# Kernel tuning notes

Measured on AMD Instinct MI355X. Metric: run time of the kernel, lower is better.

The kernel has to match this reference:

```python
import jax, jax.numpy as jnp
import numpy as np

B, NVEC, DIM, HEADS, DH, M, ITERS, DEPTH, NCLASS, KER = 8, 4096, 512, 8, 64, 256, 6, 2, 10, 33
INNER = HEADS * DH


def _ln(x, g, b, eps=1e-5):
    mu = x.mean(-1, keepdims=True)
    var = ((x - mu) ** 2).mean(-1, keepdims=True)
    return (x - mu) * jax.lax.rsqrt(var + eps) * g + b


def _mp_pinv(x, iters=ITERS):
    # Moore-Penrose pseudo-inverse via Newton-Schulz iterations (lucidrains).
    # x: [b, h, m, m]
    abs_x = jnp.abs(x)
    col = abs_x.sum(-1).max(-1)  # [b, h]
    row = abs_x.sum(-2).max(-1)  # [b, h]
    z = jnp.swapaxes(x, -1, -2) / (col * row)[..., None, None]
    I = jnp.eye(x.shape[-1], dtype=x.dtype)
    for _ in range(iters):
        xz = x @ z
        z = 0.25 * z @ (13.0 * I - xz @ (15.0 * I - xz @ (7.0 * I - xz)))
    return z


def _nystrom_attn(x, qkv_w, out_w, out_b, conv_w):
    b, n, _ = x.shape
    qkv = x @ qkv_w  # [b, n, 3*inner]
    q, k, v = jnp.split(qkv, 3, axis=-1)
    to_h = lambda t: t.reshape(b, n, HEADS, DH).transpose(0, 2, 1, 3)  # [b,h,n,dh]
    q, k, v = to_h(q), to_h(k), to_h(v)
    q = q * (DH ** -0.5)

    l = n // M  # tokens per landmark segment (n divisible by M)
    q_l = q.reshape(b, HEADS, M, l, DH).mean(3)  # [b,h,M,dh]
    k_l = k.reshape(b, HEADS, M, l, DH).mean(3)

    attn1 = jax.nn.softmax(jnp.einsum('bhnd,bhmd->bhnm', q, k_l), axis=-1)    # [b,h,n,M]
    attn2 = jax.nn.softmax(jnp.einsum('bhmd,bhld->bhml', q_l, k_l), axis=-1)  # [b,h,M,M]
    attn3 = jax.nn.softmax(jnp.einsum('bhmd,bhnd->bhmn', q_l, k), axis=-1)    # [b,h,M,n]

    out = (attn1 @ _mp_pinv(attn2)) @ (attn3 @ v)  # [b,h,n,dh]

    # residual depthwise conv over sequence dim (kernel 33, groups=heads, no bias)
    out = out + jax.lax.conv_general_dilated(
        v, conv_w, (1, 1), [(KER // 2, KER // 2), (0, 0)],
        dimension_numbers=('NCHW', 'OIHW', 'NCHW'), feature_group_count=HEADS)

    out = out.transpose(0, 2, 1, 3).reshape(b, n, INNER)
    return out @ out_w + out_b


def setup_inputs():
    key = jax.random.key(0)
    ks = jax.random.split(key, 12)
    s = 0.02
    f32 = jnp.float32
    return {
        'x': jax.random.normal(ks[0], (B, NVEC, 2), f32),
        'lin_w': jax.random.normal(ks[1], (2, DIM), f32) * s,
        'lin_b': jnp.zeros((DIM,), f32),
        'ln1_g': jnp.ones((DEPTH, DIM), f32),
        'ln1_b': jnp.zeros((DEPTH, DIM), f32),
        'qkv_w': jax.random.normal(ks[2], (DEPTH, DIM, 3 * INNER), f32) * s,
        'out_w': jax.random.normal(ks[3], (DEPTH, INNER, DIM), f32) * s,
        'out_b': jnp.zeros((DEPTH, DIM), f32),
        'conv_w': jax.random.normal(ks[4], (DEPTH, HEADS, 1, KER, 1), f32) * s,
        'ln2_g': jnp.ones((DEPTH, DIM), f32),
        'ln2_b': jnp.zeros((DEPTH, DIM), f32),
        'ff1_w': jax.random.normal(ks[5], (DEPTH, DIM, 4 * DIM), f32) * s,
        'ff1_b': jnp.zeros((DEPTH, 4 * DIM), f32),
        'ff2_w': jax.random.normal(ks[6], (DEPTH, 4 * DIM, DIM), f32) * s,
        'ff2_b': jnp.zeros((DEPTH, DIM), f32),
        'final_w': jax.random.normal(ks[7], (NVEC * DIM, NCLASS), f32) * s,
        'final_b': jnp.zeros((NCLASS,), f32),
    }


def reference(x, lin_w, lin_b, ln1_g, ln1_b, qkv_w, out_w, out_b, conv_w,
              ln2_g, ln2_b, ff1_w, ff1_b, ff2_w, ff2_b, final_w, final_b):
    h = x @ lin_w + lin_b  # [B, NVEC, DIM]
    for i in range(DEPTH):
        h = h + _nystrom_attn(_ln(h, ln1_g[i], ln1_b[i]), qkv_w[i], out_w[i], out_b[i], conv_w[i])
        z = _ln(h, ln2_g[i], ln2_b[i])
        h = h + (jax.nn.gelu(z @ ff1_w[i] + ff1_b[i]) @ ff2_w[i] + ff2_b[i])
    return h.reshape(h.shape[0], -1) @ final_w + final_b  # [B, NCLASS]
```

## Files before the change

### kernel.cpp

```cpp
#include <hip/hip_runtime.h>
#include <hip/hip_bf16.h>

#define BB_ 8
#define NVEC 4096
#define DIM 512
#define HEADS 8
#define DH 64
#define MM_ 256
#define ITERS 6
#define DEPTH 2
#define NCLASS 10
#define KER 33
#define INNER 512
#define LSEG 16

typedef long long ll;
typedef __bf16 bh16;
typedef __attribute__((ext_vector_type(8))) __bf16 bf16x8;
typedef __attribute__((ext_vector_type(4))) float f32x4;

template<int WR, int WC, bool TRB, bool GELU_ACT, bool RESID, bool BF16OUT,
         bool DUAL, bool SMAX>
__global__ void __launch_bounds__(256)
mgemm_k(const bh16* __restrict__ A, const bh16* __restrict__ B,
        const float* __restrict__ bias, void* __restrict__ Cv, void* __restrict__ C2v,
        int K, int lda, int ldb, int ldc,
        int BI, ll sAo, ll sAi, ll sBo, ll sBi, ll sCo, ll sCi,
        float alpha, float diagv)
{
    constexpr int BM = WR * 64, BN = WC * 64;
    const int bz = blockIdx.z;
    const int bo = bz / BI, bi = bz % BI;
    const bh16* Ab = A + bo * sAo + (ll)bi * sAi;
    const bh16* Bb = B + bo * sBo + (ll)bi * sBi;
    const ll coff = bo * sCo + (ll)bi * sCi;

    const int gx = gridDim.x;
    const int nwg = gx * gridDim.y;
    int flat = blockIdx.y * gx + blockIdx.x;
    {
        int xcd = flat & 7, base = flat >> 3;
        int q = nwg >> 3, rr = nwg & 7;
        flat = (xcd < rr ? xcd * (q + 1) : rr * (q + 1) + (xcd - rr) * q) + base;
    }
    const int m0 = (flat / gx) * BM;
    const int n0 = (flat % gx) * BN;

    const int tid = threadIdx.x;
    const int lane = tid & 63;
    const int wave = tid >> 6;
    const int wr = wave / WC, wc = wave % WC;

    __shared__ bh16 Al[BM * 32];
    __shared__ bh16 Bl[BN * 32];
    __shared__ float srow[SMAX ? 4 * 64 : 4];

    f32x4 acc[4][4];
#pragma unroll
    for (int i = 0; i < 4; ++i)
#pragma unroll
        for (int j = 0; j < 4; ++j) acc[i][j] = (f32x4){0.f, 0.f, 0.f, 0.f};

    const int srowi = tid >> 2;
    const int ssl   = tid & 3;

    const int rsel  = ((lane & 15) >> 1) & 3;
    const int kslot = lane >> 4;

    for (int k0 = 0; k0 < K; k0 += 32) {
        __syncthreads();
#pragma unroll
        for (int i = 0; i < BM / 64; ++i) {
            int row = i * 64 + srowi;
            int gsl = ssl ^ ((row >> 1) & 3);
            __builtin_amdgcn_global_load_lds(
                (const __attribute__((address_space(1))) unsigned int*)
                    (Ab + (ll)(m0 + row) * lda + k0 + gsl * 8),
                (__attribute__((address_space(3))) unsigned int*)
                    (Al + row * 32 + ssl * 8),
                16, 0, 0);
        }
        if (!TRB) {
#pragma unroll
            for (int i = 0; i < BN / 64; ++i) {
                int row = i * 64 + srowi;
                int gsl = ssl ^ ((row >> 1) & 3);
                __builtin_amdgcn_global_load_lds(
                    (const __attribute__((address_space(1))) unsigned int*)
                        (Bb + (ll)(n0 + row) * ldb + k0 + gsl * 8),
                    (__attribute__((address_space(3))) unsigned int*)
                        (Bl + row * 32 + ssl * 8),
                    16, 0, 0);
            }
        } else {
            const int bk = tid >> 3;
            const int nb0 = (tid & 7) * (BN / 8);
#pragma unroll
            for (int v8 = 0; v8 < BN / 64; ++v8) {
                int nb = nb0 + v8 * 8;
                bf16x8 v = *(const bf16x8*)(Bb + (ll)(k0 + bk) * ldb + n0 + nb);
#pragma unroll
                for (int j = 0; j < 8; ++j) {
                    int n = nb + j;
                    int sl = (bk >> 3) ^ ((n >> 1) & 3);
                    Bl[n * 32 + sl * 8 + (bk & 7)] = v[j];
                }
            }
        }
        __syncthreads();

        bf16x8 af[4], bfr[4];
#pragma unroll
        for (int mi = 0; mi < 4; ++mi) {
            int row = wr * 64 + mi * 16 + (lane & 15);
            af[mi] = *(const bf16x8*)(Al + row * 32 + (kslot ^ rsel) * 8);
        }
#pragma unroll
        for (int ni = 0; ni < 4; ++ni) {
            int row = wc * 64 + ni * 16 + (lane & 15);
            bfr[ni] = *(const bf16x8*)(Bl + row * 32 + (kslot ^ rsel) * 8);
        }
#pragma unroll
        for (int mi = 0; mi < 4; ++mi)
#pragma unroll
            for (int ni = 0; ni < 4; ++ni)
                acc[mi][ni] = __builtin_amdgcn_mfma_f32_16x16x32_bf16(
                    af[mi], bfr[ni], acc[mi][ni], 0, 0, 0);
    }

    if (SMAX) {
        bh16* Cb = (bh16*)Cv;
#pragma unroll
        for (int mi = 0; mi < 4; ++mi)
#pragma unroll
            for (int ni = 0; ni < 4; ++ni)
#pragma unroll
                for (int r = 0; r < 4; ++r) acc[mi][ni][r] *= alpha;
        float mx[4][4];
#pragma unroll
        for (int mi = 0; mi < 4; ++mi)
#pragma unroll
            for (int r = 0; r < 4; ++r) {
                float m_ = acc[mi][0][r];
#pragma unroll
                for (int ni = 1; ni < 4; ++ni) m_ = fmaxf(m_, acc[mi][ni][r]);
#pragma unroll
                for (int msk = 1; msk < 16; msk <<= 1)
                    m_ = fmaxf(m_, __shfl_xor(m_, msk));
                mx[mi][r] = m_;
            }
        if ((lane & 15) == 0) {
#pragma unroll
            for (int mi = 0; mi < 4; ++mi)
#pragma unroll
                for (int r = 0; r < 4; ++r)
                    srow[wc * 64 + mi * 16 + (lane >> 4) * 4 + r] = mx[mi][r];
        }
        __syncthreads();
        float M_[4][4];
#pragma unroll
        for (int mi = 0; mi < 4; ++mi)
#pragma unroll
            for (int r = 0; r < 4; ++r) {
                int row = mi * 16 + (lane >> 4) * 4 + r;
                M_[mi][r] = fmaxf(fmaxf(srow[row], srow[64 + row]),
                                  fmaxf(srow[128 + row], srow[192 + row]));
            }
        __syncthreads();
        float sm[4][4];
#pragma unroll
        for (int mi = 0; mi < 4; ++mi)
#pragma unroll
            for (int r = 0; r < 4; ++r) {
                float s_ = 0.f;
#pragma unroll
                for (int ni = 0; ni < 4; ++ni) {
                    float e = __expf(acc[mi][ni][r] - M_[mi][r]);
                    acc[mi][ni][r] = e;
                    s_ += e;
                }
#pragma unroll
                for (int msk = 1; msk < 16; msk <<= 1)
                    s_ += __shfl_xor(s_, msk);
                sm[mi][r] = s_;
            }
        if ((lane & 15) == 0) {
#pragma unroll
            for (int mi = 0; mi < 4; ++mi)
#pragma unroll
                for (int r = 0; r < 4; ++r)
                    srow[wc * 64 + mi * 16 + (lane >> 4) * 4 + r] = sm[mi][r];
        }
        __syncthreads();
#pragma unroll
        for (int mi = 0; mi < 4; ++mi)
#pragma unroll
            for (int r = 0; r < 4; ++r) {
                int row = mi * 16 + (lane >> 4) * 4 + r;
                float inv = 1.0f / (srow[row] + srow[64 + row] +
                                    srow[128 + row] + srow[192 + row]);
                int rowg = m0 + row;
#pragma unroll
                for (int ni = 0; ni < 4; ++ni) {
                    int colg = n0 + wc * 64 + ni * 16 + (lane & 15);
                    Cb[coff + (ll)rowg * ldc + colg] = (bh16)(acc[mi][ni][r] * inv);
                }
            }
        return;
    }

#pragma unroll
    for (int mi = 0; mi < 4; ++mi) {
#pragma unroll
        for (int ni = 0; ni < 4; ++ni) {
            const int colg = n0 + wc * 64 + ni * 16 + (lane & 15);
            const float bia = (!DUAL && bias) ? bias[colg] : 0.f;
#pragma unroll
            for (int r = 0; r < 4; ++r) {
                const int rowg = m0 + wr * 64 + mi * 16 + (lane >> 4) * 4 + r;
                const float a = acc[mi][ni][r];
                const ll off = coff + (ll)rowg * ldc + colg;
                if (DUAL) {
                    ((bh16*)Cv)[off] = (bh16)a;
                    float w = ((rowg == colg) ? diagv : 0.f) - a;
                    ((bh16*)C2v)[off] = (bh16)w;
                } else {
                    float v = alpha * a + bia;
                    if (diagv != 0.f && rowg == colg) v += diagv;
                    if (GELU_ACT) {
                        float t = tanhf(0.7978845608f * (v + 0.044715f * v * v * v));
                        v = 0.5f * v * (1.0f + t);
                    }
                    if (BF16OUT) {
                        ((bh16*)Cv)[off] = (bh16)v;
                    } else {
                        float* p = (float*)Cv + off;
                        float o = v;
                        if (RESID) o += *p;
                        *p = o;
                    }
                }
            }
        }
    }
}

template<int WR, int WC, bool TRB, bool G, bool R, bool BO, bool D, bool SX>
static inline void mg(hipStream_t s, int M, int N, int K,
                      const bh16* A, int lda, const bh16* B, int ldb,
                      void* C, int ldc, void* C2, const float* bias,
                      int batch, int BI,
                      ll sAo, ll sAi, ll sBo, ll sBi, ll sCo, ll sCi,
                      float alpha, float diagv)
{
    dim3 grid(N / (WC * 64), M / (WR * 64), batch);
    hipLaunchKernelGGL((mgemm_k<WR, WC, TRB, G, R, BO, D, SX>), grid, dim3(256), 0, s,
                       A, B, bias, C, C2, K, lda, ldb, ldc, BI,
                       sAo, sAi, sBo, sBi, sCo, sCi, alpha, diagv);
}

__global__ void __launch_bounds__(256)
fattn_k(const bh16* __restrict__ qkv, const bh16* __restrict__ klb,
        const bh16* __restrict__ wbt, bh16* __restrict__ aout)
{
    const int qb = blockIdx.x;
    const int bh = blockIdx.y;
    const int b = bh >> 3, h = bh & 7;
    const int q0 = qb * 64;
    const int tid = threadIdx.x, lane = tid & 63, wave = tid >> 6;
    const ll SMPq = (ll)NVEC * 1536;

    __shared__ bh16 Pl[64 * 256];
    __shared__ float red[64 * 64];
    float* srow = red;

    const bh16* qbase = qkv + (ll)b * SMPq + (ll)q0 * 1536 + h * 64;
    const bh16* klbh = klb + (ll)bh * 16384;
    const bh16* wbh  = wbt + (ll)bh * 16384;

    const int kslot = lane >> 4;

    f32x4 acc[4][4];
#pragma unroll
    for (int i = 0; i < 4; ++i)
#pragma unroll
        for (int j = 0; j < 4; ++j) acc[i][j] = (f32x4){0.f, 0.f, 0.f, 0.f};
#pragma unroll
    for (int ks = 0; ks < 2; ++ks) {
        int k0 = ks * 32;
        bf16x8 af[4], bfr[4];
#pragma unroll
        for (int mi = 0; mi < 4; ++mi) {
            int row = mi * 16 + (lane & 15);
            af[mi] = *(const bf16x8*)(qbase + (ll)row * 1536 + k0 + kslot * 8);
        }
#pragma unroll
        for (int ni = 0; ni < 4; ++ni) {
            int brow = wave * 64 + ni * 16 + (lane & 15);
            bfr[ni] = *(const bf16x8*)(klbh + brow * 64 + k0 + kslot * 8);
        }
#pragma unroll
        for (int mi = 0; mi < 4; ++mi)
#pragma unroll
            for (int ni = 0; ni < 4; ++ni)
                acc[mi][ni] = __builtin_amdgcn_mfma_f32_16x16x32_bf16(
                    af[mi], bfr[ni], acc[mi][ni], 0, 0, 0);
    }

#pragma unroll
    for (int mi = 0; mi < 4; ++mi)
#pragma unroll
        for (int ni = 0; ni < 4; ++ni)
#pragma unroll
            for (int r = 0; r < 4; ++r) acc[mi][ni][r] *= 0.125f;
    float mx[4][4];
#pragma unroll
    for (int mi = 0; mi < 4; ++mi)
#pragma unroll
        for (int r = 0; r < 4; ++r) {
            float m_ = acc[mi][0][r];
#pragma unroll
            for (int ni = 1; ni < 4; ++ni) m_ = fmaxf(m_, acc[mi][ni][r]);
#pragma unroll
            for (int msk = 1; msk < 16; msk <<= 1)
                m_ = fmaxf(m_, __shfl_xor(m_, msk));
            mx[mi][r] = m_;
        }
    if ((lane & 15) == 0) {
#pragma unroll
        for (int mi = 0; mi < 4; ++mi)
#pragma unroll
            for (int r = 0; r < 4; ++r)
                srow[wave * 64 + mi * 16 + (lane >> 4) * 4 + r] = mx[mi][r];
    }
    __syncthreads();
    float M_[4][4];
#pragma unroll
    for (int mi = 0; mi < 4; ++mi)
#pragma unroll
        for (int r = 0; r < 4; ++r) {
            int row = mi * 16 + (lane >> 4) * 4 + r;
            M_[mi][r] = fmaxf(fmaxf(srow[row], srow[64 + row]),
                              fmaxf(srow[128 + row], srow[192 + row]));
        }
    __syncthreads();
    float sm[4][4];
#pragma unroll
    for (int mi = 0; mi < 4; ++mi)
#pragma unroll
        for (int r = 0; r < 4; ++r) {
            float s_ = 0.f;
#pragma unroll
            for (int ni = 0; ni < 4; ++ni) {
                float e = __expf(acc[mi][ni][r] - M_[mi][r]);
                acc[mi][ni][r] = e;
                s_ += e;
            }
#pragma unroll
            for (int msk = 1; msk < 16; msk <<= 1)
                s_ += __shfl_xor(s_, msk);
            sm[mi][r] = s_;
        }
    if ((lane & 15) == 0) {
#pragma unroll
        for (int mi = 0; mi < 4; ++mi)
#pragma unroll
            for (int r = 0; r < 4; ++r)
                srow[wave * 64 + mi * 16 + (lane >> 4) * 4 + r] = sm[mi][r];
    }
    __syncthreads();
#pragma unroll
    for (int mi = 0; mi < 4; ++mi)
#pragma unroll
        for (int r = 0; r < 4; ++r) {
            int row = mi * 16 + (lane >> 4) * 4 + r;
            float inv = 1.0f / (srow[row] + srow[64 + row] +
                                srow[128 + row] + srow[192 + row]);
            int rsw = (row >> 1) & 3;
#pragma unroll
            for (int ni = 0; ni < 4; ++ni) {
                int col = wave * 64 + ni * 16 + (lane & 15);
                int kc = col >> 5, sl = (col >> 3) & 3, e = col & 7;
                Pl[row * 256 + kc * 32 + ((sl ^ rsw) * 8) + e] =
                    (bh16)(acc[mi][ni][r] * inv);
            }
        }
    __syncthreads();

    f32x4 acc2[4][4];
#pragma unroll
    for (int i = 0; i < 4; ++i)
#pragma unroll
        for (int j = 0; j < 4; ++j) acc2[i][j] = (f32x4){0.f, 0.f, 0.f, 0.f};
#pragma unroll
    for (int kk = 0; kk < 2; ++kk) {
        int k0 = wave * 64 + kk * 32;
        int kc = k0 >> 5;
        bf16x8 af[4], bfr[4];
#pragma unroll
        for (int mi = 0; mi < 4; ++mi) {
            int row = mi * 16 + (lane & 15);
            int rsw = (row >> 1) & 3;
            af[mi] = *(const bf16x8*)(Pl + row * 256 + kc * 32 + ((kslot ^ rsw) * 8));
        }
#pragma unroll
        for (int ni = 0; ni < 4; ++ni) {
            int brow = ni * 16 + (lane & 15);
            bfr[ni] = *(const bf16x8*)(wbh + brow * 256 + k0 + kslot * 8);
        }
#pragma unroll
        for (int mi = 0; mi < 4; ++mi)
#pragma unroll
            for (int ni = 0; ni < 4; ++ni)
                acc2[mi][ni] = __builtin_amdgcn_mfma_f32_16x16x32_bf16(
                    af[mi], bfr[ni], acc2[mi][ni], 0, 0, 0);
    }
    for (int w = 0; w < 4; ++w) {
        if (wave == w) {
#pragma unroll
            for (int mi = 0; mi < 4; ++mi)
#pragma unroll
                for (int ni = 0; ni < 4; ++ni)
#pragma unroll
                    for (int r = 0; r < 4; ++r) {
                        int row = mi * 16 + (lane >> 4) * 4 + r;
                        int col = ni * 16 + (lane & 15);
                        if (w == 0) red[row * 64 + col] = acc2[mi][ni][r];
                        else        red[row * 64 + col] += acc2[mi][ni][r];
                    }
        }
        __syncthreads();
    }
    {
        int flat = tid * 16;
        int row = flat >> 6, col0 = flat & 63;
        const bh16* cv = qkv + (ll)b * SMPq + (ll)(q0 + row) * 1536 + 512 + h * 64 + col0;
        bh16* op = aout + (ll)b * (NVEC * 512) + (ll)(q0 + row) * 512 + h * 64 + col0;
        bf16x8 c0 = *(const bf16x8*)cv;
        bf16x8 c1 = *(const bf16x8*)(cv + 8);
        bf16x8 o0, o1;
#pragma unroll
        for (int j = 0; j < 8; ++j) {
            o0[j] = (bh16)(red[row * 64 + col0 + j] + (float)c0[j]);
            o1[j] = (bh16)(red[row * 64 + col0 + 8 + j] + (float)c1[j]);
        }
        *(bf16x8*)op = o0;
        *(bf16x8*)(op + 8) = o1;
    }
}

__global__ void embed_k(const float* __restrict__ x, const float* __restrict__ w,
                        const float* __restrict__ b, float* __restrict__ h)
{
    ll idx = (ll)blockIdx.x * 256 + threadIdx.x;
    int d = (int)(idx & 511);
    ll bn = idx >> 9;
    h[idx] = x[bn * 2] * w[d] + x[bn * 2 + 1] * w[512 + d] + b[d];
}

__global__ void __launch_bounds__(256)
ln_k(const float* __restrict__ X, const float* __restrict__ g,
     const float* __restrict__ bta, bh16* __restrict__ Y)
{
    const ll row = blockIdx.x;
    const float* x = X + row * 512;
    bh16* y = Y + row * 512;
    const int tid = threadIdx.x;
    float v0 = x[tid], v1 = x[tid + 256];
    float s = v0 + v1;
    float q = v0 * v0 + v1 * v1;
    __shared__ float sred[8];
    for (int o = 32; o; o >>= 1) { s += __shfl_down(s, o); q += __shfl_down(q, o); }
    const int lane = tid & 63, w = tid >> 6;
    if (lane == 0) { sred[w] = s; sred[4 + w] = q; }
    __syncthreads();
    float ssum = sred[0] + sred[1] + sred[2] + sred[3];
    float qsum = sred[4] + sred[5] + sred[6] + sred[7];
    float mu = ssum * (1.0f / 512.0f);
    float var = qsum * (1.0f / 512.0f) - mu * mu;
    float r = rsqrtf(var + 1e-5f);
    y[tid] = (bh16)((v0 - mu) * r * g[tid] + bta[tid]);
    y[tid + 256] = (bh16)((v1 - mu) * r * g[tid + 256] + bta[tid + 256]);
}

__global__ void __launch_bounds__(256)
cvtT_k(const float* __restrict__ in, bh16* __restrict__ outp, int C, int R)
{
    __shared__ float t[64][65];
    const int nCt = C >> 6;
    const int c0 = (blockIdx.x % nCt) * 64;
    const int r0 = (blockIdx.x / nCt) * 64;
    const int tid = threadIdx.x;
#pragma unroll
    for (int j = 0; j < 16; ++j) {
        int idx = j * 256 + tid;
        int lr = idx >> 6, lc = idx & 63;
        t[lc][lr] = in[(ll)(r0 + lr) * C + c0 + lc];
    }
    __syncthreads();
#pragma unroll
    for (int v = 0; v < 2; ++v) {
        int flat = v * 256 + tid;
        int lc = flat >> 3, r8 = (flat & 7) * 8;
        bf16x8 o;
#pragma unroll
        for (int j = 0; j < 8; ++j) o[j] = (bh16)t[lc][r8 + j];
        *(bf16x8*)(outp + (ll)(c0 + lc) * R + r0 + r8) = o;
    }
}

__global__ void landmarks_k(const bh16* __restrict__ qkv,
                            bh16* __restrict__ qlb, bh16* __restrict__ klb)
{
    int idx = blockIdx.x * 256 + threadIdx.x;
    int d = idx & 63;
    int m = (idx >> 6) & 255;
    int h = (idx >> 14) & 7;
    int b = idx >> 17;
    const bh16* base = qkv + (ll)b * (NVEC * 1536) + (ll)(m * LSEG) * 1536 + h * 64 + d;
    float sq = 0.f, sk = 0.f;
#pragma unroll
    for (int l = 0; l < LSEG; ++l) {
        sq += (float)base[(ll)l * 1536];
        sk += (float)base[(ll)l * 1536 + 512];
    }
    ll o = (ll)(b * 8 + h) * 16384 + m * 64 + d;
    qlb[o] = (bh16)(sq * (0.0625f * 0.125f));
    klb[o] = (bh16)(sk * 0.0625f);
}

__global__ void wbt_k(const bh16* __restrict__ wb, bh16* __restrict__ wbt)
{
    int idx = blockIdx.x * 256 + threadIdx.x;
    int d = idx & 63, kg = (idx >> 6) & 31, bhh = idx >> 11;
    const bh16* p = wb + (ll)bhh * 16384 + kg * 8 * 64 + d;
    bf16x8 o;
#pragma unroll
    for (int j = 0; j < 8; ++j) o[j] = p[j * 64];
    *(bf16x8*)(wbt + (ll)bhh * 16384 + d * 256 + kg * 8) = o;
}

__global__ void a3vred_k(const float* __restrict__ part, bh16* __restrict__ outp)
{
    int idx = blockIdx.x * 256 + threadIdx.x;
    int h = idx >> 14, o = idx & 16383;
    const float* p = part + (ll)h * 131072 + o;
    float s = 0.f;
#pragma unroll
    for (int j = 0; j < 8; ++j) s += p[j * 16384];
    outp[idx] = (bh16)s;
}

__global__ void __launch_bounds__(256)
conv_k(bh16* __restrict__ qkv, const float* __restrict__ cw)
{
    int idx = blockIdx.x * 256 + threadIdx.x;
    int c8 = idx & 63;
    int ng = (idx >> 6) & 1023;
    int b  = idx >> 16;
    const int n0 = ng * 4;
    const int h = c8 >> 3;
    const bh16* v = qkv + (ll)b * (NVEC * 1536) + 1024 + c8 * 8;

    float wreg[KER];
#pragma unroll
    for (int k = 0; k < KER; ++k) wreg[k] = cw[h * KER + k];

    float acc[4][8];
#pragma unroll
    for (int t = 0; t < 4; ++t)
#pragma unroll
        for (int e = 0; e < 8; ++e) acc[t][e] = 0.f;

#pragma unroll
    for (int m = 0; m < 36; ++m) {
        int nn = n0 + m - (KER / 2);
        bf16x8 vv = {};
        if ((unsigned)nn < (unsigned)NVEC)
            vv = *(const bf16x8*)(v + (ll)nn * 1536);
#pragma unroll
        for (int t = 0; t < 4; ++t) {
            constexpr int KMAX = KER - 1;
            int k = m - t;
            if (k >= 0 && k <= KMAX) {
                float wk = wreg[k];
#pragma unroll
                for (int e = 0; e < 8; ++e)
                    acc[t][e] = fmaf((float)vv[e], wk, acc[t][e]);
            }
        }
    }

    bh16* o = qkv + (ll)b * (NVEC * 1536) + (ll)n0 * 1536 + 512 + c8 * 8;
#pragma unroll
    for (int t = 0; t < 4; ++t) {
        bf16x8 ov;
#pragma unroll
        for (int e = 0; e < 8; ++e) ov[e] = (bh16)acc[t][e];
        *(bf16x8*)(o + (ll)t * 1536) = ov;
    }
}

__device__ __forceinline__ float blkmax(float m, float* red, int tid)
{
#pragma unroll
    for (int o = 32; o; o >>= 1) m = fmaxf(m, __shfl_down(m, o));
    if ((tid & 63) == 0) red[tid >> 6] = m;
    __syncthreads();
    m = fmaxf(fmaxf(red[0], red[1]), fmaxf(red[2], red[3]));
    __syncthreads();
    return m;
}
__device__ __forceinline__ float blksum(float s, float* red, int tid)
{
#pragma unroll
    for (int o = 32; o; o >>= 1) s += __shfl_down(s, o);
    if ((tid & 63) == 0) red[tid >> 6] = s;
    __syncthreads();
    s = red[0] + red[1] + red[2] + red[3];
    __syncthreads();
    return s;
}

__global__ void __launch_bounds__(256)
softmax_f2b_k(float* __restrict__ X)
{
    const ll row = blockIdx.x;
    float* x = X + row * 4096;
    const int tid = threadIdx.x;
    __shared__ float red[4];
    float v[16];
#pragma unroll
    for (int j = 0; j < 4; ++j) {
        float4 t = *(const float4*)(x + tid * 16 + j * 4);
        v[j * 4 + 0] = t.x; v[j * 4 + 1] = t.y; v[j * 4 + 2] = t.z; v[j * 4 + 3] = t.w;
    }
    float m = -1e30f;
#pragma unroll
    for (int j = 0; j < 16; ++j) m = fmaxf(m, v[j]);
    m = blkmax(m, red, tid);
    float s = 0.f;
#pragma unroll
    for (int j = 0; j < 16; ++j) { v[j] = __expf(v[j] - m); s += v[j]; }
    s = blksum(s, red, tid);
    float inv = 1.0f / s;
    __syncthreads();
    bh16* o = (bh16*)x;
    bf16x8 oa, ob;
#pragma unroll
    for (int j = 0; j < 8; ++j) { oa[j] = (bh16)(v[j] * inv); ob[j] = (bh16)(v[8 + j] * inv); }
    *(bf16x8*)(o + tid * 16) = oa;
    *(bf16x8*)(o + tid * 16 + 8) = ob;
}

__global__ void __launch_bounds__(256)
pinv_init_k(const bh16* __restrict__ X, bh16* __restrict__ Z)
{
    const ll bh = blockIdx.x;
    const bh16* x = X + bh * 65536;
    bh16* z = Z + bh * 65536;
    const int tid = threadIdx.x;
    float rs = 0.f, cs = 0.f;
    for (int j = 0; j < 256; ++j) {
        rs += fabsf((float)x[tid * 256 + j]);
        cs += fabsf((float)x[j * 256 + tid]);
    }
    __shared__ float rbuf[256], cbuf[256];
    rbuf[tid] = rs; cbuf[tid] = cs;
    __syncthreads();
    for (int o = 128; o; o >>= 1) {
        if (tid < o) {
            rbuf[tid] = fmaxf(rbuf[tid], rbuf[tid + o]);
            cbuf[tid] = fmaxf(cbuf[tid], cbuf[tid + o]);
        }
        __syncthreads();
    }
    float inv = 1.0f / (rbuf[0] * cbuf[0]);
    for (int e = tid; e < 65536; e += 256) {
        int i = e >> 8, j = e & 255;
        z[e] = (bh16)((float)x[j * 256 + i] * inv);
    }
}

__global__ void final_init_k(const float* __restrict__ fb, float* __restrict__ out)
{
    int i = threadIdx.x;
    if (i < BB_ * NCLASS) out[i] = fb[i % NCLASS];
}

__global__ void __launch_bounds__(256)
final_gemv_k(const float* __restrict__ hbuf, const float* __restrict__ w,
             float* __restrict__ out)
{
    const int half = blockIdx.y;
    const int chunk = blockIdx.x;
    const int tid = threadIdx.x;
    const int k0 = chunk * 8192;
    float pc[4][NCLASS] = {};
    for (int e = 0; e < 32; ++e) {
        int k = k0 + e * 256 + tid;
        const float* wr = w + (ll)k * NCLASS;
        float wv[NCLASS];
#pragma unroll
        for (int c = 0; c < NCLASS; ++c) wv[c] = wr[c];
#pragma unroll
        for (int b = 0; b < 4; ++b) {
            float hv = hbuf[(ll)(half * 4 + b) * (NVEC * DIM) + k];
#pragma unroll
            for (int c = 0; c < NCLASS; ++c) pc[b][c] = fmaf(hv, wv[c], pc[b][c]);
        }
    }
    __shared__ float red[4][4][NCLASS];
    const int lane = tid & 63, wv_ = tid >> 6;
#pragma unroll
    for (int b = 0; b < 4; ++b)
#pragma unroll
        for (int c = 0; c < NCLASS; ++c) {
            float s = pc[b][c];
#pragma unroll
            for (int o = 32; o; o >>= 1) s += __shfl_down(s, o);
            if (lane == 0) red[wv_][b][c] = s;
        }
    __syncthreads();
    if (tid < 4 * NCLASS) {
        int b = tid / NCLASS, c = tid % NCLASS;
        float s = red[0][b][c] + red[1][b][c] + red[2][b][c] + red[3][b][c];
        atomicAdd(out + (half * 4 + b) * NCLASS + c, s);
    }
}

extern "C" void kernel_launch(void* const* d_in, const int* in_sizes, int n_in,
                              void* d_out, int out_size, void* d_ws, size_t ws_size,
                              hipStream_t stream)
{
    const float* x      = (const float*)d_in[0];
    const float* lin_w  = (const float*)d_in[1];
    const float* lin_b  = (const float*)d_in[2];
    const float* ln1_g  = (const float*)d_in[3];
    const float* ln1_b  = (const float*)d_in[4];
    const float* qkv_w  = (const float*)d_in[5];
    const float* out_w  = (const float*)d_in[6];
    const float* out_b  = (const float*)d_in[7];
    const float* conv_w = (const float*)d_in[8];
    const float* ln2_g  = (const float*)d_in[9];
    const float* ln2_b  = (const float*)d_in[10];
    const float* ff1_w  = (const float*)d_in[11];
    const float* ff1_b  = (const float*)d_in[12];
    const float* ff2_w  = (const float*)d_in[13];
    const float* ff2_b  = (const float*)d_in[14];
    const float* final_w = (const float*)d_in[15];
    const float* final_b = (const float*)d_in[16];
    float* out = (float*)d_out;
    float* ws  = (float*)d_ws;

    float* H    = ws;
    bh16*  QKV  = (bh16*)(ws + 16777216);
    float* P    = ws + 41943040;
    bh16*  qlbf = (bh16*)(ws + 52428800);
    bh16*  klbf = (bh16*)(ws + 52953088);
    bh16*  A3Vb = (bh16*)(ws + 53477376);
    bh16*  WBb  = (bh16*)(ws + 54001664);
    bh16*  WBT  = (bh16*)(ws + 54525952);
    bh16*  WQT  = (bh16*)(ws + 55050240);
    bh16*  WOT  = (bh16*)(ws + 55443456);
    bh16*  F1WT = (bh16*)(ws + 55574528);
    bh16*  F2WT = (bh16*)(ws + 56098816);
    if (ws_size < 56623104ULL * 4) return;

    bh16*  XLNall = (bh16*)P;
    float* SCORESf = P;
    float* A3Vp   = P + 8388608;
    bh16*  Xbf = (bh16*)P;
    bh16*  Z0  = (bh16*)(P + 2097152);
    bh16*  Z1  = (bh16*)(P + 4194304);
    bh16*  T1  = (bh16*)(P + 6291456);
    bh16*  T2  = (bh16*)(P + 8388608);
    bh16*  AOUTa  = (bh16*)P;
    bh16*  XLNc   = (bh16*)P;
    bh16*  HIDc   = (bh16*)(P + 2097152);

    const ll SMP = (ll)NVEC * 1536;

    hipLaunchKernelGGL(embed_k, dim3(65536), dim3(256), 0, stream, x, lin_w, lin_b, H);

    for (int i = 0; i < DEPTH; ++i) {
        const float* wq  = qkv_w + (ll)i * 512 * 1536;
        const float* wo  = out_w + (ll)i * 512 * 512;
        const float* bo  = out_b + (ll)i * 512;
        const float* cw  = conv_w + (ll)i * HEADS * KER;
        const float* g1  = ln1_g + (ll)i * 512;
        const float* b1  = ln1_b + (ll)i * 512;
        const float* g2  = ln2_g + (ll)i * 512;
        const float* b2  = ln2_b + (ll)i * 512;
        const float* f1w = ff1_w + (ll)i * 512 * 2048;
        const float* f1b = ff1_b + (ll)i * 2048;
        const float* f2w = ff2_w + (ll)i * 2048 * 512;
        const float* f2b = ff2_b + (ll)i * 512;

        hipLaunchKernelGGL(cvtT_k, dim3(192), dim3(256), 0, stream, wq, WQT, 1536, 512);
        hipLaunchKernelGGL(cvtT_k, dim3(64), dim3(256), 0, stream, wo, WOT, 512, 512);
        hipLaunchKernelGGL(cvtT_k, dim3(256), dim3(256), 0, stream, f1w, F1WT, 2048, 512);
        hipLaunchKernelGGL(cvtT_k, dim3(256), dim3(256), 0, stream, f2w, F2WT, 512, 2048);

        hipLaunchKernelGGL(ln_k, dim3(32768), dim3(256), 0, stream, H, g1, b1, XLNall);
        mg<2,2,0,0,0,1,0,0>(stream, 32768, 1536, 512, XLNall, 512, WQT, 512,
            QKV, 1536, nullptr, nullptr, 1, 1, 0,0, 0,0, 0,0, 1.f, 0.f);

        hipLaunchKernelGGL(landmarks_k, dim3(4096), dim3(256), 0, stream, QKV, qlbf, klbf);

        for (int b = 0; b < BB_; ++b) {
            const bh16* qkvb = QKV + (ll)b * SMP;
            mg<2,2,0,0,0,0,0,0>(stream, 256, 4096, 64,
                qlbf + (ll)b * 131072, 64, qkvb + 512, 1536,
                SCORESf, 4096, nullptr, nullptr, 8, 8,
                0, 16384, 0, 64, 0, 1048576, 1.f, 0.f);
            hipLaunchKernelGGL(softmax_f2b_k, dim3(2048), dim3(256), 0, stream, SCORESf);
            mg<4,1,1,0,0,0,0,0>(stream, 256, 64, 512,
                (const bh16*)SCORESf, 8192, qkvb + 1024, 1536,
                A3Vp, 64, nullptr, nullptr, 64, 8,
                2097152, 512, 64, 512LL * 1536, 131072, 16384, 1.f, 0.f);
            hipLaunchKernelGGL(a3vred_k, dim3(512), dim3(256), 0, stream,
                               A3Vp, A3Vb + (ll)b * 131072);
        }

        hipLaunchKernelGGL(conv_k, dim3(2048), dim3(256), 0, stream, QKV, cw);

        mg<1,4,0,0,0,1,0,1>(stream, 256, 256, 64, qlbf, 64, klbf, 64,
            Xbf, 256, nullptr, nullptr, 64, 64, 0, 16384, 0, 16384, 0, 65536, 1.f, 0.f);
        hipLaunchKernelGGL(pinv_init_k, dim3(64), dim3(256), 0, stream, Xbf, Z0);
        bh16* zc = Z0; bh16* zn = Z1;
        for (int it = 0; it < ITERS; ++it) {
            mg<2,2,1,0,0,1,1,0>(stream, 256, 256, 256, Xbf, 256, zc, 256,
                T1, 256, T2, nullptr, 64, 64, 0, 65536, 0, 65536, 0, 65536, 1.f, 7.f);
            mg<2,2,1,0,0,1,0,0>(stream, 256, 256, 256, T1, 256, T2, 256,
                zn, 256, nullptr, nullptr, 64, 64, 0, 65536, 0, 65536, 0, 65536, -1.f, 15.f);
            mg<2,2,1,0,0,1,0,0>(stream, 256, 256, 256, T1, 256, zn, 256,
                T2, 256, nullptr, nullptr, 64, 64, 0, 65536, 0, 65536, 0, 65536, -1.f, 13.f);
            mg<2,2,1,0,0,1,0,0>(stream, 256, 256, 256, zc, 256, T2, 256,
                zn, 256, nullptr, nullptr, 64, 64, 0, 65536, 0, 65536, 0, 65536, 0.25f, 0.f);
            bh16* t = zc; zc = zn; zn = t;
        }
        mg<4,1,1,0,0,1,0,0>(stream, 256, 64, 256, zc, 256, A3Vb, 64,
            WBb, 64, nullptr, nullptr, 64, 64, 0, 65536, 0, 16384, 0, 16384, 1.f, 0.f);
        hipLaunchKernelGGL(wbt_k, dim3(512), dim3(256), 0, stream, WBb, WBT);

        hipLaunchKernelGGL(fattn_k, dim3(64, 64), dim3(256), 0, stream,
                           QKV, klbf, WBT, AOUTa);
        mg<2,2,0,0,1,0,0,0>(stream, 32768, 512, 512, AOUTa, 512, WOT, 512,
            H, 512, nullptr, bo, 1, 1, 0,0, 0,0, 0,0, 1.f, 0.f);

        for (int c = 0; c < 4; ++c) {
            float* Hc = H + (ll)c * 2 * 2097152;
            hipLaunchKernelGGL(ln_k, dim3(8192), dim3(256), 0, stream, Hc, g2, b2, XLNc);
            mg<2,2,0,1,0,1,0,0>(stream, 8192, 2048, 512, XLNc, 512, F1WT, 512,
                HIDc, 2048, nullptr, f1b, 1, 1, 0,0, 0,0, 0,0, 1.f, 0.f);
            mg<2,2,0,0,1,0,0,0>(stream, 8192, 512, 2048, HIDc, 2048, F2WT, 2048,
                Hc, 512, nullptr, f2b, 1, 1, 0,0, 0,0, 0,0, 1.f, 0.f);
        }
    }

    hipLaunchKernelGGL(final_init_k, dim3(1), dim3(128), 0, stream, final_b, out);
    hipLaunchKernelGGL(final_gemv_k, dim3(256, 2), dim3(256), 0, stream, H, final_w, out);
}
```

Before: 3.317 ms.

## Split second attention GEMM by rows per wave, removing cross-wave reduction

The second MFMA stage in the fused attention kernel now has each wave own 16 output rows over the full K=256, instead of each wave computing a K-slice over all 64 rows. This removes the serialized four-step shared-memory reduction and its barriers. The P tile uses a padded pitch instead of an XOR swizzle. The epilogue now writes scalar bf16 values straight from registers, giving up the vectorized 16-byte loads and stores and adding more global memory transactions.

```diff
diff --git a/kernel.cpp b/kernel.cpp
--- a/kernel.cpp
+++ b/kernel.cpp
@@ -259,6 +259,7 @@
                        sAo, sAi, sBo, sBi, sCo, sCi, alpha, diagv);
 }
 
+#define PPITCH 264
 __global__ void __launch_bounds__(256)
 fattn_k(const bh16* __restrict__ qkv, const bh16* __restrict__ klb,
         const bh16* __restrict__ wbt, bh16* __restrict__ aout)
@@ -270,9 +271,8 @@
     const int tid = threadIdx.x, lane = tid & 63, wave = tid >> 6;
     const ll SMPq = (ll)NVEC * 1536;
 
-    __shared__ bh16 Pl[64 * 256];
-    __shared__ float red[64 * 64];
-    float* srow = red;
+    __shared__ bh16 Pl[64 * PPITCH];
+    __shared__ float srow[256];
 
     const bh16* qbase = qkv + (ll)b * SMPq + (ll)q0 * 1536 + h * 64;
     const bh16* klbh = klb + (ll)bh * 16384;
@@ -376,76 +376,45 @@
             int row = mi * 16 + (lane >> 4) * 4 + r;
             float inv = 1.0f / (srow[row] + srow[64 + row] +
                                 srow[128 + row] + srow[192 + row]);
-            int rsw = (row >> 1) & 3;
 #pragma unroll
             for (int ni = 0; ni < 4; ++ni) {
                 int col = wave * 64 + ni * 16 + (lane & 15);
-                int kc = col >> 5, sl = (col >> 3) & 3, e = col & 7;
-                Pl[row * 256 + kc * 32 + ((sl ^ rsw) * 8) + e] =
-                    (bh16)(acc[mi][ni][r] * inv);
-            }
-        }
-    __syncthreads();
-
-    f32x4 acc2[4][4];
-#pragma unroll
-    for (int i = 0; i < 4; ++i)
-#pragma unroll
-        for (int j = 0; j < 4; ++j) acc2[i][j] = (f32x4){0.f, 0.f, 0.f, 0.f};
-#pragma unroll
-    for (int kk = 0; kk < 2; ++kk) {
-        int k0 = wave * 64 + kk * 32;
-        int kc = k0 >> 5;
-        bf16x8 af[4], bfr[4];
-#pragma unroll
-        for (int mi = 0; mi < 4; ++mi) {
-            int row = mi * 16 + (lane & 15);
-            int rsw = (row >> 1) & 3;
-            af[mi] = *(const bf16x8*)(Pl + row * 256 + kc * 32 + ((kslot ^ rsw) * 8));
-        }
+                Pl[row * PPITCH + col] = (bh16)(acc[mi][ni][r] * inv);
+            }
+        }
+    __syncthreads();
+
+    f32x4 acc2[4];
+#pragma unroll
+    for (int j = 0; j < 4; ++j) acc2[j] = (f32x4){0.f, 0.f, 0.f, 0.f};
+    const int arow = wave * 16 + (lane & 15);
+#pragma unroll
+    for (int ks = 0; ks < 8; ++ks) {
+        int k0 = ks * 32;
+        bf16x8 af = *(const bf16x8*)(Pl + arow * PPITCH + k0 + kslot * 8);
+        bf16x8 bfr[4];
 #pragma unroll
         for (int ni = 0; ni < 4; ++ni) {
             int brow = ni * 16 + (lane & 15);
             bfr[ni] = *(const bf16x8*)(wbh + brow * 256 + k0 + kslot * 8);
         }
 #pragma unroll
-        for (int mi = 0; mi < 4; ++mi)
-#pragma unroll
-            for (int ni = 0; ni < 4; ++ni)
-                acc2[mi][ni] = __builtin_amdgcn_mfma_f32_16x16x32_bf16(
-                    af[mi], bfr[ni], acc2[mi][ni], 0, 0, 0);
-    }
-    for (int w = 0; w < 4; ++w) {
-        if (wave == w) {
-#pragma unroll
-            for (int mi = 0; mi < 4; ++mi)
-#pragma unroll
-                for (int ni = 0; ni < 4; ++ni)
-#pragma unroll
-                    for (int r = 0; r < 4; ++r) {
-                        int row = mi * 16 + (lane >> 4) * 4 + r;
-                        int col = ni * 16 + (lane & 15);
-                        if (w == 0) red[row * 64 + col] = acc2[mi][ni][r];
-                        else        red[row * 64 + col] += acc2[mi][ni][r];
-                    }
-        }
-        __syncthreads();
-    }
-    {
-        int flat = tid * 16;
-        int row = flat >> 6, col0 = flat & 63;
-        const bh16* cv = qkv + (ll)b * SMPq + (ll)(q0 + row) * 1536 + 512 + h * 64 + col0;
-        bh16* op = aout + (ll)b * (NVEC * 512) + (ll)(q0 + row) * 512 + h * 64 + col0;
-        bf16x8 c0 = *(const bf16x8*)cv;
-        bf16x8 c1 = *(const bf16x8*)(cv + 8);
-        bf16x8 o0, o1;
-#pragma unroll
-        for (int j = 0; j < 8; ++j) {
-            o0[j] = (bh16)(red[row * 64 + col0 + j] + (float)c0[j]);
-            o1[j] = (bh16)(red[row * 64 + col0 + 8 + j] + (float)c1[j]);
-        }
-        *(bf16x8*)op = o0;
-        *(bf16x8*)(op + 8) = o1;
+        for (int ni = 0; ni < 4; ++ni)
+            acc2[ni] = __builtin_amdgcn_mfma_f32_16x16x32_bf16(
+                af, bfr[ni], acc2[ni], 0, 0, 0);
+    }
+
+#pragma unroll
+    for (int ni = 0; ni < 4; ++ni) {
+        const int col = ni * 16 + (lane & 15);
+#pragma unroll
+        for (int r = 0; r < 4; ++r) {
+            const int row = wave * 16 + (lane >> 4) * 4 + r;
+            const ll nrow = (ll)(q0 + row);
+            float cv = (float)qkv[(ll)b * SMPq + nrow * 1536 + 512 + h * 64 + col];
+            aout[(ll)b * (NVEC * 512) + nrow * 512 + h * 64 + col] =
+                (bh16)(acc2[ni][r] + cv);
+        }
     }
 }
 
```

Result: no change. 3.333 ms (+0.5%).

## Batch attn3 over sample pairs with bf16 scores and padded fattn shared memory

Applied to the files above, without the earlier changes.

The per-sample loop for the attn3 path now processes two samples per iteration. The score GEMM writes bf16 directly instead of fp32, and the softmax reads and writes bf16 in place. This halves score-buffer traffic and reduces launch count, with the reduction kernel covering both samples. In fattn_k, the XOR-swizzled P tile becomes a padded-pitch layout that shares one buffer with the reduction scratch, separated by an extra barrier. This lowers LDS footprint, which may raise occupancy, at the cost of an added sync.

```diff
diff --git a/kernel.cpp b/kernel.cpp
--- a/kernel.cpp
+++ b/kernel.cpp
@@ -259,6 +259,8 @@
                        sAo, sAi, sBo, sBi, sCo, sCi, alpha, diagv);
 }
 
+#define PPITCH 264
+#define RPITCH 68
 __global__ void __launch_bounds__(256)
 fattn_k(const bh16* __restrict__ qkv, const bh16* __restrict__ klb,
         const bh16* __restrict__ wbt, bh16* __restrict__ aout)
@@ -270,9 +272,10 @@
     const int tid = threadIdx.x, lane = tid & 63, wave = tid >> 6;
     const ll SMPq = (ll)NVEC * 1536;
 
-    __shared__ bh16 Pl[64 * 256];
-    __shared__ float red[64 * 64];
-    float* srow = red;
+    __shared__ __align__(16) char smem[64 * PPITCH * 2];
+    bh16*  Pl  = (bh16*)smem;
+    float* red = (float*)smem;
+    __shared__ float srow[256];
 
     const bh16* qbase = qkv + (ll)b * SMPq + (ll)q0 * 1536 + h * 64;
     const bh16* klbh = klb + (ll)bh * 16384;
@@ -376,13 +379,10 @@
             int row = mi * 16 + (lane >> 4) * 4 + r;
             float inv = 1.0f / (srow[row] + srow[64 + row] +
                                 srow[128 + row] + srow[192 + row]);
-            int rsw = (row >> 1) & 3;
 #pragma unroll
             for (int ni = 0; ni < 4; ++ni) {
                 int col = wave * 64 + ni * 16 + (lane & 15);
-                int kc = col >> 5, sl = (col >> 3) & 3, e = col & 7;
-                Pl[row * 256 + kc * 32 + ((sl ^ rsw) * 8) + e] =
-                    (bh16)(acc[mi][ni][r] * inv);
+                Pl[row * PPITCH + col] = (bh16)(acc[mi][ni][r] * inv);
             }
         }
     __syncthreads();
@@ -395,13 +395,11 @@
 #pragma unroll
     for (int kk = 0; kk < 2; ++kk) {
         int k0 = wave * 64 + kk * 32;
-        int kc = k0 >> 5;
         bf16x8 af[4], bfr[4];
 #pragma unroll
         for (int mi = 0; mi < 4; ++mi) {
             int row = mi * 16 + (lane & 15);
-            int rsw = (row >> 1) & 3;
-            af[mi] = *(const bf16x8*)(Pl + row * 256 + kc * 32 + ((kslot ^ rsw) * 8));
+            af[mi] = *(const bf16x8*)(Pl + row * PPITCH + k0 + kslot * 8);
         }
 #pragma unroll
         for (int ni = 0; ni < 4; ++ni) {
@@ -415,6 +413,8 @@
                 acc2[mi][ni] = __builtin_amdgcn_mfma_f32_16x16x32_bf16(
                     af[mi], bfr[ni], acc2[mi][ni], 0, 0, 0);
     }
+    __syncthreads();
+
     for (int w = 0; w < 4; ++w) {
         if (wave == w) {
 #pragma unroll
@@ -425,24 +425,26 @@
                     for (int r = 0; r < 4; ++r) {
                         int row = mi * 16 + (lane >> 4) * 4 + r;
                         int col = ni * 16 + (lane & 15);
-                        if (w == 0) red[row * 64 + col] = acc2[mi][ni][r];
-                        else        red[row * 64 + col] += acc2[mi][ni][r];
+                        if (w == 0) red[row * RPITCH + col] = acc2[mi][ni][r];
+                        else        red[row * RPITCH + col] += acc2[mi][ni][r];
                     }
         }
         __syncthreads();
     }
+
     {
-        int flat = tid * 16;
-        int row = flat >> 6, col0 = flat & 63;
-        const bh16* cv = qkv + (ll)b * SMPq + (ll)(q0 + row) * 1536 + 512 + h * 64 + col0;
-        bh16* op = aout + (ll)b * (NVEC * 512) + (ll)(q0 + row) * 512 + h * 64 + col0;
+        const int row = tid >> 2;
+        const int col0 = (tid & 3) * 16;
+        const ll nrow = (ll)(q0 + row);
+        const bh16* cv = qkv + (ll)b * SMPq + nrow * 1536 + 512 + h * 64 + col0;
+        bh16* op = aout + (ll)b * (NVEC * 512) + nrow * 512 + h * 64 + col0;
         bf16x8 c0 = *(const bf16x8*)cv;
         bf16x8 c1 = *(const bf16x8*)(cv + 8);
         bf16x8 o0, o1;
 #pragma unroll
         for (int j = 0; j < 8; ++j) {
-            o0[j] = (bh16)(red[row * 64 + col0 + j] + (float)c0[j]);
-            o1[j] = (bh16)(red[row * 64 + col0 + 8 + j] + (float)c1[j]);
+            o0[j] = (bh16)(red[row * RPITCH + col0 + j] + (float)c0[j]);
+            o1[j] = (bh16)(red[row * RPITCH + col0 + 8 + j] + (float)c1[j]);
         }
         *(bf16x8*)op = o0;
         *(bf16x8*)(op + 8) = o1;
@@ -543,12 +545,14 @@
 __global__ void a3vred_k(const float* __restrict__ part, bh16* __restrict__ outp)
 {
     int idx = blockIdx.x * 256 + threadIdx.x;
-    int h = idx >> 14, o = idx & 16383;
-    const float* p = part + (ll)h * 131072 + o;
+    int smp = idx >> 17;
+    int rest = idx & 131071;
+    int h = rest >> 14, o = rest & 16383;
+    const float* p = part + (ll)smp * 1048576 + (ll)h * 131072 + o;
     float s = 0.f;
 #pragma unroll
     for (int j = 0; j < 8; ++j) s += p[j * 16384];
-    outp[idx] = (bh16)s;
+    outp[(ll)(smp * 8 + h) * 16384 + o] = (bh16)s;
 }
 
 __global__ void __launch_bounds__(256)
@@ -623,18 +627,17 @@
 }
 
 __global__ void __launch_bounds__(256)
-softmax_f2b_k(float* __restrict__ X)
+softmax_bf_k(bh16* __restrict__ X, int L)
 {
     const ll row = blockIdx.x;
-    float* x = X + row * 4096;
+    bh16* x = X + row * (ll)L;
     const int tid = threadIdx.x;
     __shared__ float red[4];
     float v[16];
-#pragma unroll
-    for (int j = 0; j < 4; ++j) {
-        float4 t = *(const float4*)(x + tid * 16 + j * 4);
-        v[j * 4 + 0] = t.x; v[j * 4 + 1] = t.y; v[j * 4 + 2] = t.z; v[j * 4 + 3] = t.w;
-    }
+    bf16x8 a = *(const bf16x8*)(x + tid * 8);
+    bf16x8 b = *(const bf16x8*)(x + 2048 + tid * 8);
+#pragma unroll
+    for (int j = 0; j < 8; ++j) { v[j] = (float)a[j]; v[8 + j] = (float)b[j]; }
     float m = -1e30f;
 #pragma unroll
     for (int j = 0; j < 16; ++j) m = fmaxf(m, v[j]);
@@ -644,13 +647,11 @@
     for (int j = 0; j < 16; ++j) { v[j] = __expf(v[j] - m); s += v[j]; }
     s = blksum(s, red, tid);
     float inv = 1.0f / s;
-    __syncthreads();
-    bh16* o = (bh16*)x;
     bf16x8 oa, ob;
 #pragma unroll
     for (int j = 0; j < 8; ++j) { oa[j] = (bh16)(v[j] * inv); ob[j] = (bh16)(v[8 + j] * inv); }
-    *(bf16x8*)(o + tid * 16) = oa;
-    *(bf16x8*)(o + tid * 16 + 8) = ob;
+    *(bf16x8*)(x + tid * 8) = oa;
+    *(bf16x8*)(x + 2048 + tid * 8) = ob;
 }
 
 __global__ void __launch_bounds__(256)
@@ -768,7 +769,7 @@
     if (ws_size < 56623104ULL * 4) return;
 
     bh16*  XLNall = (bh16*)P;
-    float* SCORESf = P;
+    bh16*  ATT3c  = (bh16*)P;
     float* A3Vp   = P + 8388608;
     bh16*  Xbf = (bh16*)P;
     bh16*  Z0  = (bh16*)(P + 2097152);
@@ -808,19 +809,21 @@
 
         hipLaunchKernelGGL(landmarks_k, dim3(4096), dim3(256), 0, stream, QKV, qlbf, klbf);
 
-        for (int b = 0; b < BB_; ++b) {
-            const bh16* qkvb = QKV + (ll)b * SMP;
-            mg<2,2,0,0,0,0,0,0>(stream, 256, 4096, 64,
-                qlbf + (ll)b * 131072, 64, qkvb + 512, 1536,
-                SCORESf, 4096, nullptr, nullptr, 8, 8,
-                0, 16384, 0, 64, 0, 1048576, 1.f, 0.f);
-            hipLaunchKernelGGL(softmax_f2b_k, dim3(2048), dim3(256), 0, stream, SCORESf);
-            mg<4,1,1,0,0,0,0,0>(stream, 256, 64, 512,
-                (const bh16*)SCORESf, 8192, qkvb + 1024, 1536,
-                A3Vp, 64, nullptr, nullptr, 64, 8,
-                2097152, 512, 64, 512LL * 1536, 131072, 16384, 1.f, 0.f);
-            hipLaunchKernelGGL(a3vred_k, dim3(512), dim3(256), 0, stream,
-                               A3Vp, A3Vb + (ll)b * 131072);
+        for (int c = 0; c < 4; ++c) {
+            const bh16* qkvc = QKV + (ll)c * 2 * SMP;
+            mg<2,2,0,0,0,1,0,0>(stream, 256, 4096, 64,
+                qlbf + (ll)c * 262144, 64, qkvc + 512, 1536,
+                ATT3c, 4096, nullptr, nullptr, 16, 8,
+                131072, 16384, SMP, 64, 8388608LL, 1048576, 1.f, 0.f);
+            hipLaunchKernelGGL(softmax_bf_k, dim3(4096), dim3(256), 0, stream, ATT3c, 4096);
+            for (int s = 0; s < 2; ++s) {
+                mg<4,1,1,0,0,0,0,0>(stream, 256, 64, 512,
+                    ATT3c + (ll)s * 8 * 1048576, 4096, qkvc + (ll)s * SMP + 1024, 1536,
+                    A3Vp + (ll)s * 1048576, 64, nullptr, nullptr, 64, 8,
+                    1048576, 512, 64, 512LL * 1536, 131072, 16384, 1.f, 0.f);
+            }
+            hipLaunchKernelGGL(a3vred_k, dim3(1024), dim3(256), 0, stream,
+                               A3Vp, A3Vb + (ll)c * 2 * 131072);
         }
 
         hipLaunchKernelGGL(conv_k, dim3(2048), dim3(256), 0, stream, QKV, cw);
```

Result: faster. 3.179 ms, median of 2 (-4.2%).
